# Kernel optimization log

Hardware: AMD Instinct MI355X
Metric: run time of the kernel (lower is better)

## Reference

```python
import jax, jax.numpy as jnp
from jax import lax
import numpy as np

NUM_DROPS = 10
MIN_R, MAX_R = 60.0, 80.0
BETA = 1.8
# fixed (non-trainable) blur radii from the module buffer
BLUR_RADII = [11.3535, 17.9381, 5.7966, 10.8586, 5.5301, 15.9075, 12.3225, 13.4871, 6.6639, 9.5413]

def _ksize(r):
    k = int(2 * r) + 1
    return k + 1 if k % 2 == 0 else k

KSIZES = [_ksize(r) for r in BLUR_RADII]  # [23, 37, 13, 23, 13, 33, 25, 27, 15, 21]

# learned-parameter initial values from the module source
POS0 = np.array([[0.07, -0.68], [-0.83, -0.12], [0.57, -0.09], [-0.12, -0.19],
                 [-0.47, -0.12], [0.83, -0.45], [0.42, -0.62], [-0.31, -0.66],
                 [-0.71, -0.64], [0.2, -0.14]], dtype=np.float32)
RAD0 = np.array([68.9755, 66.3124, 78.3028, 64.0275, 64.5939,
                 64.1804, 61.6286, 73.2401, 66.8596, 59.9934], dtype=np.float32)


def _gaussian_blur(x, sigma, ksize):
    # torchvision GaussianBlur: separable depthwise conv, reflect padding
    half = (ksize - 1) * 0.5
    xs = jnp.linspace(-half, half, ksize)
    pdf = jnp.exp(-0.5 * (xs / sigma) ** 2)
    k1 = (pdf / pdf.sum()).astype(x.dtype)
    pad = ksize // 2
    C = x.shape[1]
    dn = ('NCHW', 'OIHW', 'NCHW')
    kv = jnp.tile(k1.reshape(1, 1, ksize, 1), (C, 1, 1, 1))
    kh = jnp.tile(k1.reshape(1, 1, 1, ksize), (C, 1, 1, 1))
    xp = jnp.pad(x, ((0, 0), (0, 0), (pad, pad), (0, 0)), mode='reflect')
    x = lax.conv_general_dilated(xp, kv, (1, 1), 'VALID', dimension_numbers=dn, feature_group_count=C)
    xp = jnp.pad(x, ((0, 0), (0, 0), (0, 0), (pad, pad)), mode='reflect')
    x = lax.conv_general_dilated(xp, kh, (1, 1), 'VALID', dimension_numbers=dn, feature_group_count=C)
    return x


def setup_inputs() -> dict:
    key = jax.random.key(0)
    img = jax.random.uniform(key, (16, 3, 768, 768), dtype=jnp.float32)
    positions = jnp.asarray(POS0)
    radius = jnp.asarray(RAD0)
    return {"img": img, "positions": positions, "radius": radius}


def reference(img, positions, radius):
    B, C, H, W = img.shape
    pos = jnp.clip(positions, -1.0, 1.0)
    rad = jnp.clip(radius, MIN_R, MAX_R)
    hv = jnp.arange(H, dtype=img.dtype)[:, None]  # [H,1]
    wv = jnp.arange(W, dtype=img.dtype)[None, :]  # [1,W]
    out = img
    # drops are identical across the batch, so process whole batch per drop
    for j in range(NUM_DROPS):
        x0 = (pos[j, 0] + 1.0) / 2.0 * W
        y0 = (pos[j, 1] + 1.0) / 2.0 * H
        wr = rad[j]
        hr = wr * 0.8
        d = (hv - y0) ** 2 / hr ** 2 + (wv - x0) ** 2 / wr ** 2  # [H,W]
        mask = jnp.clip(jnp.exp(-(d ** BETA) + 1e-10), 0.0, 1.0)
        blurred = _gaussian_blur(out * mask[None, None], BLUR_RADII[j], KSIZES[j])
        out = blurred * mask[None, None] + out * (1.0 - mask[None, None])
    return out
```

## Files before the change

kernel.cpp:

```cpp
#include <hip/hip_runtime.h>
#include <cmath>

namespace {

constexpr int B = 16, C = 3, H = 768, W = 768;
constexpr int HW = H * W;
constexpr int BC = B * C;
constexpr int NDROPS = 10;
constexpr int KS[NDROPS] = {23, 37, 13, 23, 13, 33, 25, 27, 15, 21};
constexpr float BLUR_R[NDROPS] = {11.3535f, 17.9381f, 5.7966f, 10.8586f, 5.5301f,
                                  15.9075f, 12.3225f, 13.4871f, 6.6639f, 9.5413f};
constexpr int MAXK = 37;
constexpr int MAXP = MAXK / 2;

constexpr float SFAC = 2.17f;
constexpr int BOXW = 384;
constexpr int BOXH = 288;
constexpr int YT = 32;
constexpr int MH = BOXH + 2 * MAXP;
constexpr int MW = 448;

struct TapW {
    float w[MAXK];
};

}

__device__ inline int refl(int v, int n) {
    return v < 0 ? -v : (v >= n ? 2 * n - 2 - v : v);
}

__device__ inline void drop_params(const float* __restrict__ pos,
                                   const float* __restrict__ rad, int j,
                                   float& x0, float& y0, float& wr, float& hr) {
    float px = fminf(fmaxf(pos[2 * j + 0], -1.f), 1.f);
    float py = fminf(fmaxf(pos[2 * j + 1], -1.f), 1.f);
    wr = fminf(fmaxf(rad[j], 60.f), 80.f);
    x0 = (px + 1.f) * 0.5f * (float)W;
    y0 = (py + 1.f) * 0.5f * (float)H;
    hr = wr * 0.8f;
}

__device__ inline void drop_box(const float* __restrict__ pos,
                                const float* __restrict__ rad, int j,
                                int& bx0, int& by0) {
    float x0, y0, wr, hr;
    drop_params(pos, rad, j, x0, y0, wr, hr);
    bx0 = max(0, (int)floorf(x0 - SFAC * wr));
    by0 = max(0, (int)floorf(y0 - SFAC * hr));
}

__global__ void maskbox_kernel(const float* __restrict__ pos,
                               const float* __restrict__ rad,
                               float* __restrict__ mbox) {
    int j = blockIdx.y;
    int idx = blockIdx.x * 256 + threadIdx.x;
    if (idx >= MH * MW) return;
    int yi = idx / MW;
    int xi = idx - yi * MW;
    int bx0, by0;
    drop_box(pos, rad, j, bx0, by0);
    float x0, y0, wr, hr;
    drop_params(pos, rad, j, x0, y0, wr, hr);
    int rx = refl(bx0 - MAXP + xi, W);
    int ry = refl(by0 - MAXP + yi, H);
    float dy = (float)ry - y0;
    float dx = (float)rx - x0;
    float d = dy * dy / (hr * hr) + dx * dx / (wr * wr);
    float m = expf(-powf(d, 1.8f) + 1e-10f);
    m = fminf(fmaxf(m, 0.f), 1.f);
    mbox[(size_t)j * MH * MW + idx] = m;
}

__global__ void copy_kernel(const float4* __restrict__ src,
                            float4* __restrict__ dst, int n) {
    int i = blockIdx.x * blockDim.x + threadIdx.x;
    if (i < n) dst[i] = src[i];
}

template <int K>
__global__ __launch_bounds__(256) void fusedDrop(
    const float* __restrict__ out, const float* __restrict__ mbox,
    float* __restrict__ stage, const float* __restrict__ pos,
    const float* __restrict__ rad, int j, TapW tw) {
    constexpr int P = K / 2;
    constexpr int TC = 64 + K - 1;
    constexpr int TR = YT + K - 1;
    constexpr int PC = TC + 2;
    constexpr int VC = TC + 1;
    __shared__ float prod[TR][PC];
    __shared__ float vbl[YT][VC];

    int bx0, by0;
    drop_box(pos, rad, j, bx0, by0);
    int tx = threadIdx.x, ty = threadIdx.y;
    int xb = blockIdx.x * 64;
    int yb = blockIdx.y * YT;
    int bc = blockIdx.z;
    const float* mb = mbox + (size_t)j * MH * MW;
    const float* op = out + (size_t)bc * HW;

    for (int cc = tx; cc < TC; cc += 64) {
        int rx = refl(bx0 + xb - P + cc, W);
        int xim = xb + cc + (MAXP - P);
        for (int r = ty; r < TR; r += 4) {
            int ry = refl(by0 + yb - P + r, H);
            prod[r][cc] = op[ry * W + rx] * mb[(yb + r + (MAXP - P)) * MW + xim];
        }
    }
    __syncthreads();

    {
        int c0 = 2 * tx;
        int base = ty * 8;
        if (c0 < TC) {
            float a0[8] = {0, 0, 0, 0, 0, 0, 0, 0};
            float a1[8] = {0, 0, 0, 0, 0, 0, 0, 0};
#pragma unroll
            for (int t = 0; t < K + 7; ++t) {
                float2 v = *(const float2*)&prod[base + t][c0];
#pragma unroll
                for (int o = 0; o < 8; ++o) {
                    int ti = t - o;
                    if (ti >= 0 && ti < K) {
                        a0[o] += tw.w[ti] * v.x;
                        a1[o] += tw.w[ti] * v.y;
                    }
                }
            }
#pragma unroll
            for (int o = 0; o < 8; ++o) {
                vbl[base + o][c0] = a0[o];
                vbl[base + o][c0 + 1] = a1[o];
            }
        }
    }
    __syncthreads();

    {
        int tid = ty * 64 + tx;
        int xq = (tid & 7) * 8;
        int yi = tid >> 3;
        float acc[8] = {0, 0, 0, 0, 0, 0, 0, 0};
#pragma unroll
        for (int t = 0; t < K + 7; ++t) {
            float v = vbl[yi][xq + t];
#pragma unroll
            for (int o = 0; o < 8; ++o) {
                int ti = t - o;
                if (ti >= 0 && ti < K) acc[o] += tw.w[ti] * v;
            }
        }
        float* srow = stage + ((size_t)bc * BOXH + (yb + yi)) * BOXW + (xb + xq);
        *(float4*)&srow[0] = make_float4(acc[0], acc[1], acc[2], acc[3]);
        *(float4*)&srow[4] = make_float4(acc[4], acc[5], acc[6], acc[7]);
    }
}

__global__ __launch_bounds__(256) void composite_kernel(
    const float* __restrict__ stage, const float* __restrict__ mbox,
    float* __restrict__ out, const float* __restrict__ pos,
    const float* __restrict__ rad, int j) {
    int bx0, by0;
    drop_box(pos, rad, j, bx0, by0);
    int ci = blockIdx.x * 64 + threadIdx.x;
    int yi = blockIdx.y * 4 + threadIdx.y;
    int bc = blockIdx.z;
    int x = bx0 + ci;
    int y = by0 + yi;
    if (x >= W || y >= H) return;
    float m = mbox[(size_t)j * MH * MW + (size_t)(yi + MAXP) * MW + (ci + MAXP)];
    float s = stage[((size_t)bc * BOXH + yi) * BOXW + ci];
    size_t o = (size_t)bc * HW + (size_t)y * W + x;
    out[o] = s * m + out[o] * (1.f - m);
}

static void make_weights(int j, TapW& tw) {
    int K = KS[j];
    float sigma = BLUR_R[j];
    float half = (K - 1) * 0.5f;
    float sum = 0.f;
    for (int i = 0; i < K; ++i) {
        float xx = -half + (float)i;
        float v = xx / sigma;
        float p = expf(-0.5f * v * v);
        tw.w[i] = p;
        sum += p;
    }
    for (int i = 0; i < K; ++i) tw.w[i] /= sum;
    for (int i = K; i < MAXK; ++i) tw.w[i] = 0.f;
}

template <int K>
static void launch_fused(hipStream_t stream, const float* out,
                         const float* mbox, float* stage, const float* pos,
                         const float* rad, int j, const TapW& tw) {
    dim3 blk(64, 4, 1);
    dim3 grid(BOXW / 64, BOXH / YT, BC);
    fusedDrop<K><<<grid, blk, 0, stream>>>(out, mbox, stage, pos, rad, j, tw);
}

static void launch_drop(int K, hipStream_t stream, float* out,
                        const float* mbox, float* stage, const float* pos,
                        const float* rad, int j, const TapW& tw) {
    switch (K) {
        case 13: launch_fused<13>(stream, out, mbox, stage, pos, rad, j, tw); break;
        case 15: launch_fused<15>(stream, out, mbox, stage, pos, rad, j, tw); break;
        case 21: launch_fused<21>(stream, out, mbox, stage, pos, rad, j, tw); break;
        case 23: launch_fused<23>(stream, out, mbox, stage, pos, rad, j, tw); break;
        case 25: launch_fused<25>(stream, out, mbox, stage, pos, rad, j, tw); break;
        case 27: launch_fused<27>(stream, out, mbox, stage, pos, rad, j, tw); break;
        case 33: launch_fused<33>(stream, out, mbox, stage, pos, rad, j, tw); break;
        case 37: launch_fused<37>(stream, out, mbox, stage, pos, rad, j, tw); break;
    }
    dim3 blk(64, 4, 1);
    dim3 grid(BOXW / 64, BOXH / 4, BC);
    composite_kernel<<<grid, blk, 0, stream>>>(stage, mbox, out, pos, rad, j);
}

extern "C" void kernel_launch(void* const* d_in, const int* in_sizes, int n_in,
                              void* d_out, int out_size, void* d_ws,
                              size_t ws_size, hipStream_t stream) {
    const float* img = (const float*)d_in[0];
    const float* pos = (const float*)d_in[1];
    const float* rad = (const float*)d_in[2];
    float* out = (float*)d_out;

    float* mbox = (float*)d_ws;
    float* stage = mbox + (size_t)NDROPS * MH * MW;

    maskbox_kernel<<<dim3((MH * MW + 255) / 256, NDROPS), 256, 0, stream>>>(
        pos, rad, mbox);
    copy_kernel<<<(BC * HW / 4 + 255) / 256, 256, 0, stream>>>(
        (const float4*)img, (float4*)out, BC * HW / 4);

    for (int j = 0; j < NDROPS; ++j) {
        TapW tw;
        make_weights(j, tw);
        launch_drop(KS[j], stream, out, mbox, stage, pos, rad, j, tw);
    }
}
```

Before: 690.1 us.

## Merge all drop passes into one persistent cooperative kernel with grid syncs

```diff
diff --git a/kernel.cpp b/kernel.cpp
--- a/kernel.cpp
+++ b/kernel.cpp
@@ -1,5 +1,8 @@
 #include <hip/hip_runtime.h>
+#include <hip/hip_cooperative_groups.h>
 #include <cmath>
+
+namespace cg = cooperative_groups;
 
 namespace {
 
@@ -19,9 +22,16 @@
 constexpr int YT = 32;
 constexpr int MH = BOXH + 2 * MAXP;
 constexpr int MW = 448;
-
-struct TapW {
-    float w[MAXK];
+constexpr int NXT = BOXW / 64;
+constexpr int NYT = BOXH / YT;
+constexpr int NTILES = NXT * NYT * BC;
+
+constexpr int PSTR = 64 + MAXK - 1 + 2;
+constexpr int VSTR = 64 + MAXK - 1 + 1;
+constexpr int PROWS = YT + MAXK - 1;
+
+struct AllW {
+    float w[NDROPS][MAXK];
 };
 
 }
@@ -50,132 +60,162 @@
     by0 = max(0, (int)floorf(y0 - SFAC * hr));
 }
 
-__global__ void maskbox_kernel(const float* __restrict__ pos,
-                               const float* __restrict__ rad,
-                               float* __restrict__ mbox) {
-    int j = blockIdx.y;
-    int idx = blockIdx.x * 256 + threadIdx.x;
-    if (idx >= MH * MW) return;
-    int yi = idx / MW;
-    int xi = idx - yi * MW;
-    int bx0, by0;
-    drop_box(pos, rad, j, bx0, by0);
-    float x0, y0, wr, hr;
-    drop_params(pos, rad, j, x0, y0, wr, hr);
-    int rx = refl(bx0 - MAXP + xi, W);
-    int ry = refl(by0 - MAXP + yi, H);
-    float dy = (float)ry - y0;
-    float dx = (float)rx - x0;
-    float d = dy * dy / (hr * hr) + dx * dx / (wr * wr);
-    float m = expf(-powf(d, 1.8f) + 1e-10f);
-    m = fminf(fmaxf(m, 0.f), 1.f);
-    mbox[(size_t)j * MH * MW + idx] = m;
-}
-
-__global__ void copy_kernel(const float4* __restrict__ src,
-                            float4* __restrict__ dst, int n) {
-    int i = blockIdx.x * blockDim.x + threadIdx.x;
-    if (i < n) dst[i] = src[i];
-}
-
 template <int K>
-__global__ __launch_bounds__(256) void fusedDrop(
-    const float* __restrict__ out, const float* __restrict__ mbox,
-    float* __restrict__ stage, const float* __restrict__ pos,
-    const float* __restrict__ rad, int j, TapW tw) {
+__device__ void do_drop(const float* __restrict__ wrow,
+                        const float* __restrict__ mb, float* __restrict__ out,
+                        float* __restrict__ stage,
+                        const float* __restrict__ pos,
+                        const float* __restrict__ rad, int j,
+                        float* __restrict__ prod_s, float* __restrict__ vbl_s) {
     constexpr int P = K / 2;
     constexpr int TC = 64 + K - 1;
     constexpr int TR = YT + K - 1;
-    constexpr int PC = TC + 2;
-    constexpr int VC = TC + 1;
-    __shared__ float prod[TR][PC];
-    __shared__ float vbl[YT][VC];
-
     int bx0, by0;
     drop_box(pos, rad, j, bx0, by0);
-    int tx = threadIdx.x, ty = threadIdx.y;
-    int xb = blockIdx.x * 64;
-    int yb = blockIdx.y * YT;
-    int bc = blockIdx.z;
-    const float* mb = mbox + (size_t)j * MH * MW;
-    const float* op = out + (size_t)bc * HW;
-
-    for (int cc = tx; cc < TC; cc += 64) {
-        int rx = refl(bx0 + xb - P + cc, W);
-        int xim = xb + cc + (MAXP - P);
-        for (int r = ty; r < TR; r += 4) {
-            int ry = refl(by0 + yb - P + r, H);
-            prod[r][cc] = op[ry * W + rx] * mb[(yb + r + (MAXP - P)) * MW + xim];
-        }
-    }
-    __syncthreads();
-
-    {
-        int c0 = 2 * tx;
-        int base = ty * 8;
-        if (c0 < TC) {
-            float a0[8] = {0, 0, 0, 0, 0, 0, 0, 0};
-            float a1[8] = {0, 0, 0, 0, 0, 0, 0, 0};
+    const int tx = threadIdx.x, ty = threadIdx.y;
+
+    for (int tile = blockIdx.x; tile < NTILES; tile += gridDim.x) {
+        int xt = tile % NXT;
+        int r6 = tile / NXT;
+        int yt = r6 % NYT;
+        int bc = r6 / NYT;
+        int xb = xt * 64, yb = yt * YT;
+        const float* op = out + (size_t)bc * HW;
+
+        for (int cc = tx; cc < TC; cc += 64) {
+            int rx = refl(bx0 + xb - P + cc, W);
+            int xim = xb + cc + (MAXP - P);
+            for (int r = ty; r < TR; r += 4) {
+                int ry = refl(by0 + yb - P + r, H);
+                prod_s[r * PSTR + cc] =
+                    op[ry * W + rx] * mb[(yb + r + (MAXP - P)) * MW + xim];
+            }
+        }
+        __syncthreads();
+
+        {
+            int c0 = 2 * tx;
+            int base = ty * 8;
+            if (c0 < TC) {
+                float a0[8] = {0, 0, 0, 0, 0, 0, 0, 0};
+                float a1[8] = {0, 0, 0, 0, 0, 0, 0, 0};
+#pragma unroll
+                for (int t = 0; t < K + 7; ++t) {
+                    float2 v = *(const float2*)&prod_s[(base + t) * PSTR + c0];
+#pragma unroll
+                    for (int o = 0; o < 8; ++o) {
+                        int ti = t - o;
+                        if (ti >= 0 && ti < K) {
+                            a0[o] += wrow[ti] * v.x;
+                            a1[o] += wrow[ti] * v.y;
+                        }
+                    }
+                }
+#pragma unroll
+                for (int o = 0; o < 8; ++o) {
+                    vbl_s[(base + o) * VSTR + c0] = a0[o];
+                    vbl_s[(base + o) * VSTR + c0 + 1] = a1[o];
+                }
+            }
+        }
+        __syncthreads();
+
+        {
+            int tid = ty * 64 + tx;
+            int xq = (tid & 7) * 8;
+            int yi = tid >> 3;
+            float acc[8] = {0, 0, 0, 0, 0, 0, 0, 0};
 #pragma unroll
             for (int t = 0; t < K + 7; ++t) {
-                float2 v = *(const float2*)&prod[base + t][c0];
+                float v = vbl_s[yi * VSTR + xq + t];
 #pragma unroll
                 for (int o = 0; o < 8; ++o) {
                     int ti = t - o;
-                    if (ti >= 0 && ti < K) {
-                        a0[o] += tw.w[ti] * v.x;
-                        a1[o] += tw.w[ti] * v.y;
-                    }
-                }
-            }
+                    if (ti >= 0 && ti < K) acc[o] += wrow[ti] * v;
+                }
+            }
+            float* srow =
+                stage + ((size_t)bc * BOXH + (yb + yi)) * BOXW + (xb + xq);
+            *(float4*)&srow[0] = make_float4(acc[0], acc[1], acc[2], acc[3]);
+            *(float4*)&srow[4] = make_float4(acc[4], acc[5], acc[6], acc[7]);
+        }
+        __syncthreads();
+    }
+    cg::this_grid().sync();
+
+    for (int tile = blockIdx.x; tile < NTILES; tile += gridDim.x) {
+        int xt = tile % NXT;
+        int r6 = tile / NXT;
+        int yt = r6 % NYT;
+        int bc = r6 / NYT;
+        int ci = xt * 64 + tx;
+        int x = bx0 + ci;
+        if (x < W) {
 #pragma unroll
             for (int o = 0; o < 8; ++o) {
-                vbl[base + o][c0] = a0[o];
-                vbl[base + o][c0 + 1] = a1[o];
-            }
-        }
-    }
-    __syncthreads();
+                int yi = yt * YT + ty * 8 + o;
+                int y = by0 + yi;
+                if (y < H) {
+                    float m = mb[(size_t)(yi + MAXP) * MW + (ci + MAXP)];
+                    float s = stage[((size_t)bc * BOXH + yi) * BOXW + ci];
+                    size_t oo = (size_t)bc * HW + (size_t)y * W + x;
+                    out[oo] = s * m + out[oo] * (1.f - m);
+                }
+            }
+        }
+    }
+    cg::this_grid().sync();
+}
+
+__global__ __launch_bounds__(256) void condensation_all(
+    const float* __restrict__ img, const float* __restrict__ pos,
+    const float* __restrict__ rad, float* __restrict__ out,
+    float* __restrict__ mbox, float* __restrict__ stage, AllW allw) {
+    __shared__ float prod_s[PROWS * PSTR];
+    __shared__ float vbl_s[YT * VSTR];
+
+    const int tid = threadIdx.y * 64 + threadIdx.x;
+    const int gtid = blockIdx.x * 256 + tid;
+    const int gstride = gridDim.x * 256;
 
     {
-        int tid = ty * 64 + tx;
-        int xq = (tid & 7) * 8;
-        int yi = tid >> 3;
-        float acc[8] = {0, 0, 0, 0, 0, 0, 0, 0};
-#pragma unroll
-        for (int t = 0; t < K + 7; ++t) {
-            float v = vbl[yi][xq + t];
-#pragma unroll
-            for (int o = 0; o < 8; ++o) {
-                int ti = t - o;
-                if (ti >= 0 && ti < K) acc[o] += tw.w[ti] * v;
-            }
-        }
-        float* srow = stage + ((size_t)bc * BOXH + (yb + yi)) * BOXW + (xb + xq);
-        *(float4*)&srow[0] = make_float4(acc[0], acc[1], acc[2], acc[3]);
-        *(float4*)&srow[4] = make_float4(acc[4], acc[5], acc[6], acc[7]);
-    }
-}
-
-__global__ __launch_bounds__(256) void composite_kernel(
-    const float* __restrict__ stage, const float* __restrict__ mbox,
-    float* __restrict__ out, const float* __restrict__ pos,
-    const float* __restrict__ rad, int j) {
-    int bx0, by0;
-    drop_box(pos, rad, j, bx0, by0);
-    int ci = blockIdx.x * 64 + threadIdx.x;
-    int yi = blockIdx.y * 4 + threadIdx.y;
-    int bc = blockIdx.z;
-    int x = bx0 + ci;
-    int y = by0 + yi;
-    if (x >= W || y >= H) return;
-    float m = mbox[(size_t)j * MH * MW + (size_t)(yi + MAXP) * MW + (ci + MAXP)];
-    float s = stage[((size_t)bc * BOXH + yi) * BOXW + ci];
-    size_t o = (size_t)bc * HW + (size_t)y * W + x;
-    out[o] = s * m + out[o] * (1.f - m);
-}
-
-static void make_weights(int j, TapW& tw) {
+        const float4* s4 = (const float4*)img;
+        float4* d4 = (float4*)out;
+        for (int i = gtid; i < BC * HW / 4; i += gstride) d4[i] = s4[i];
+    }
+    for (int idx = gtid; idx < NDROPS * MH * MW; idx += gstride) {
+        int j = idx / (MH * MW);
+        int rem = idx - j * (MH * MW);
+        int yi = rem / MW;
+        int xi = rem - yi * MW;
+        int bx0, by0;
+        drop_box(pos, rad, j, bx0, by0);
+        float x0, y0, wr, hr;
+        drop_params(pos, rad, j, x0, y0, wr, hr);
+        int rx = refl(bx0 - MAXP + xi, W);
+        int ry = refl(by0 - MAXP + yi, H);
+        float dy = (float)ry - y0;
+        float dx = (float)rx - x0;
+        float d = dy * dy / (hr * hr) + dx * dx / (wr * wr);
+        float m = expf(-powf(d, 1.8f) + 1e-10f);
+        m = fminf(fmaxf(m, 0.f), 1.f);
+        mbox[idx] = m;
+    }
+    cg::this_grid().sync();
+
+    do_drop<KS[0]>(allw.w[0], mbox + 0 * (size_t)MH * MW, out, stage, pos, rad, 0, prod_s, vbl_s);
+    do_drop<KS[1]>(allw.w[1], mbox + 1 * (size_t)MH * MW, out, stage, pos, rad, 1, prod_s, vbl_s);
+    do_drop<KS[2]>(allw.w[2], mbox + 2 * (size_t)MH * MW, out, stage, pos, rad, 2, prod_s, vbl_s);
+    do_drop<KS[3]>(allw.w[3], mbox + 3 * (size_t)MH * MW, out, stage, pos, rad, 3, prod_s, vbl_s);
+    do_drop<KS[4]>(allw.w[4], mbox + 4 * (size_t)MH * MW, out, stage, pos, rad, 4, prod_s, vbl_s);
+    do_drop<KS[5]>(allw.w[5], mbox + 5 * (size_t)MH * MW, out, stage, pos, rad, 5, prod_s, vbl_s);
+    do_drop<KS[6]>(allw.w[6], mbox + 6 * (size_t)MH * MW, out, stage, pos, rad, 6, prod_s, vbl_s);
+    do_drop<KS[7]>(allw.w[7], mbox + 7 * (size_t)MH * MW, out, stage, pos, rad, 7, prod_s, vbl_s);
+    do_drop<KS[8]>(allw.w[8], mbox + 8 * (size_t)MH * MW, out, stage, pos, rad, 8, prod_s, vbl_s);
+    do_drop<KS[9]>(allw.w[9], mbox + 9 * (size_t)MH * MW, out, stage, pos, rad, 9, prod_s, vbl_s);
+}
+
+static void make_weights(int j, float* w) {
     int K = KS[j];
     float sigma = BLUR_R[j];
     float half = (K - 1) * 0.5f;
@@ -184,38 +224,11 @@
         float xx = -half + (float)i;
         float v = xx / sigma;
         float p = expf(-0.5f * v * v);
-        tw.w[i] = p;
+        w[i] = p;
         sum += p;
     }
-    for (int i = 0; i < K; ++i) tw.w[i] /= sum;
-    for (int i = K; i < MAXK; ++i) tw.w[i] = 0.f;
-}
-
-template <int K>
-static void launch_fused(hipStream_t stream, const float* out,
-                         const float* mbox, float* stage, const float* pos,
-                         const float* rad, int j, const TapW& tw) {
-    dim3 blk(64, 4, 1);
-    dim3 grid(BOXW / 64, BOXH / YT, BC);
-    fusedDrop<K><<<grid, blk, 0, stream>>>(out, mbox, stage, pos, rad, j, tw);
-}
-
-static void launch_drop(int K, hipStream_t stream, float* out,
-                        const float* mbox, float* stage, const float* pos,
-                        const float* rad, int j, const TapW& tw) {
-    switch (K) {
-        case 13: launch_fused<13>(stream, out, mbox, stage, pos, rad, j, tw); break;
-        case 15: launch_fused<15>(stream, out, mbox, stage, pos, rad, j, tw); break;
-        case 21: launch_fused<21>(stream, out, mbox, stage, pos, rad, j, tw); break;
-        case 23: launch_fused<23>(stream, out, mbox, stage, pos, rad, j, tw); break;
-        case 25: launch_fused<25>(stream, out, mbox, stage, pos, rad, j, tw); break;
-        case 27: launch_fused<27>(stream, out, mbox, stage, pos, rad, j, tw); break;
-        case 33: launch_fused<33>(stream, out, mbox, stage, pos, rad, j, tw); break;
-        case 37: launch_fused<37>(stream, out, mbox, stage, pos, rad, j, tw); break;
-    }
-    dim3 blk(64, 4, 1);
-    dim3 grid(BOXW / 64, BOXH / 4, BC);
-    composite_kernel<<<grid, blk, 0, stream>>>(stage, mbox, out, pos, rad, j);
+    for (int i = 0; i < K; ++i) w[i] /= sum;
+    for (int i = K; i < MAXK; ++i) w[i] = 0.f;
 }
 
 extern "C" void kernel_launch(void* const* d_in, const int* in_sizes, int n_in,
@@ -229,14 +242,23 @@
     float* mbox = (float*)d_ws;
     float* stage = mbox + (size_t)NDROPS * MH * MW;
 
-    maskbox_kernel<<<dim3((MH * MW + 255) / 256, NDROPS), 256, 0, stream>>>(
-        pos, rad, mbox);
-    copy_kernel<<<(BC * HW / 4 + 255) / 256, 256, 0, stream>>>(
-        (const float4*)img, (float4*)out, BC * HW / 4);
-
-    for (int j = 0; j < NDROPS; ++j) {
-        TapW tw;
-        make_weights(j, tw);
-        launch_drop(KS[j], stream, out, mbox, stage, pos, rad, j, tw);
-    }
-}
+    AllW allw;
+    for (int j = 0; j < NDROPS; ++j) make_weights(j, allw.w[j]);
+
+    int occ = 0;
+    (void)hipOccupancyMaxActiveBlocksPerMultiprocessor(
+        &occ, reinterpret_cast<const void*>(condensation_all), 256, 0);
+    if (occ < 1) occ = 1;
+    int dev = 0;
+    (void)hipGetDevice(&dev);
+    int cus = 256;
+    (void)hipDeviceGetAttribute(&cus, hipDeviceAttributeMultiprocessorCount, dev);
+    long grid = (long)occ * (long)cus;
+    if (grid > NTILES) grid = NTILES;
+
+    void* args[] = {(void*)&img, (void*)&pos, (void*)&rad, (void*)&out,
+                    (void*)&mbox, (void*)&stage, (void*)&allw};
+    (void)hipLaunchCooperativeKernel(
+        reinterpret_cast<const void*>(condensation_all), dim3((unsigned)grid),
+        dim3(64, 4, 1), args, 0, stream);
+}
```

After: 2.739 ms. 297% more time.
